# Kernel tuning notes

Hardware: AMD Instinct MI355X
Metric: run time of the kernel (lower is better)

Reference implementation:

```python
import jax, jax.numpy as jnp
import numpy as np

N_NODES = 100000
N_EDGES = 1600000
HIDDEN = 256
CONV_OUT = 128
OUT = 2


def setup_inputs() -> dict:
    key = jax.random.key(0)
    k1, k2, k3, k4, k5, k6, k7 = jax.random.split(key, 7)
    x = jax.random.normal(k1, (N_NODES, HIDDEN), dtype=jnp.float32)
    edge_index = jax.random.randint(k2, (2, N_EDGES), 0, N_NODES, dtype=jnp.int64)
    edge_weight = jax.random.uniform(k3, (N_EDGES,), dtype=jnp.float32)
    # GCNConv parameters (lin: hidden->128, bias added after aggregation)
    W1 = jax.random.normal(k4, (HIDDEN, CONV_OUT), dtype=jnp.float32) / np.sqrt(HIDDEN)
    b1 = jnp.zeros((CONV_OUT,), dtype=jnp.float32)
    # head Linear(128, out_channels)
    W2 = jax.random.normal(k5, (CONV_OUT, OUT), dtype=jnp.float32) / np.sqrt(CONV_OUT)
    b2 = jax.random.normal(k6, (OUT,), dtype=jnp.float32) * 0.01
    return {"x": x, "edge_index": edge_index, "edge_weight": edge_weight,
            "W1": W1, "b1": b1, "W2": W2, "b2": b2}


def reference(x, edge_index, edge_weight, W1, b1, W2, b2):
    # GCNConv (use_weights=True branch, no relu), dropout in eval mode (identity), then Linear.
    N = x.shape[0]
    src, dst = edge_index[0], edge_index[1]
    # add self-loops with weight 1 (PyG default fill_value=1.0)
    loop = jnp.arange(N, dtype=src.dtype)
    src = jnp.concatenate([src, loop])
    dst = jnp.concatenate([dst, loop])
    w = jnp.concatenate([edge_weight, jnp.ones((N,), dtype=edge_weight.dtype)])
    # symmetric normalization: norm = d^{-1/2}[src] * w * d^{-1/2}[dst]
    deg = jax.ops.segment_sum(w, dst, num_segments=N)
    dinv = jnp.where(deg > 0, jax.lax.rsqrt(deg), 0.0)
    norm = dinv[src] * w * dinv[dst]
    # transform then gather-scatter aggregate
    h = x @ W1                                   # [N, 128]
    msgs = norm[:, None] * h[src]                # [E+N, 128]
    agg = jax.ops.segment_sum(msgs, dst, num_segments=N) + b1  # [N, 128]
    return agg @ W2 + b2                         # [N, out_channels]
```

## Files before the change

### kernel.cpp

```cpp
#include <hip/hip_runtime.h>

#define N_NODES 100000
#define N_EDGES 1600000
#define HIDDEN 256

#define BSH 7
#define BNODES 128
#define NB 782
#define CAP 2560
#define NPB 200
#define EPB 8000
#define ZNPW 16
#define ZNPB 64
#define NZB 1563


__global__ __launch_bounds__(256) void k_init(
        const float* __restrict__ W1, const float* __restrict__ b1,
        const float* __restrict__ W2, const float* __restrict__ b2,
        float* __restrict__ W12, float* __restrict__ cvec, int* __restrict__ gcur) {
    if (blockIdx.x == 0) {
        int h = threadIdx.x;
        const float4* w1r = (const float4*)(W1 + (size_t)h * 128);
        float a0 = 0.f, a1 = 0.f;
#pragma unroll 8
        for (int k4 = 0; k4 < 32; ++k4) {
            float4 v = w1r[k4];
            a0 += v.x * W2[8 * k4 + 0]; a1 += v.x * W2[8 * k4 + 1];
            a0 += v.y * W2[8 * k4 + 2]; a1 += v.y * W2[8 * k4 + 3];
            a0 += v.z * W2[8 * k4 + 4]; a1 += v.z * W2[8 * k4 + 5];
            a0 += v.w * W2[8 * k4 + 6]; a1 += v.w * W2[8 * k4 + 7];
        }
        W12[2 * h] = a0; W12[2 * h + 1] = a1;
        if (h < 2) {
            float acc = b2[h];
            for (int k = 0; k < 128; ++k) acc += b1[k] * W2[2 * k + h];
            cvec[h] = acc;
        }
    } else {
        int i = (blockIdx.x - 1) * 256 + threadIdx.x;
        if (i < NB) gcur[i] = 0;
    }
}

__global__ __launch_bounds__(256) void k_main(
        const float* __restrict__ x, const int* __restrict__ ei,
        const float* __restrict__ ew, const float* __restrict__ W12,
        int* __restrict__ gcur, uint2* __restrict__ rec, float* __restrict__ z) {
    __shared__ struct { int hist[NB]; int cursor[NB]; } sm;
    const int tid = threadIdx.x, bid = blockIdx.x;
    if (bid < NPB) {
        for (int i = tid; i < NB; i += 256) sm.hist[i] = 0;
        __syncthreads();
        const int e0 = bid * EPB;
        for (int e = e0 + tid; e < e0 + EPB; e += 256)
            atomicAdd(&sm.hist[((unsigned)ei[N_EDGES + e]) >> BSH], 1);
        __syncthreads();
        for (int i = tid; i < NB; i += 256) {
            int c = sm.hist[i];
            int pos = c ? atomicAdd(&gcur[i], c) : 0;
            sm.cursor[i] = i * CAP + pos;
        }
        __syncthreads();
        for (int e = e0 + tid; e < e0 + EPB; e += 256) {
            int d = ei[N_EDGES + e];
            int s = ei[e];
            int bk = ((unsigned)d) >> BSH;
            int p = atomicAdd(&sm.cursor[bk], 1);
            if (p < (bk + 1) * CAP)
                rec[p] = make_uint2((unsigned)s | ((unsigned)(d & (BNODES - 1)) << 17),
                                    __float_as_uint(ew[e]));
        }
    } else {
        const int lane = tid & 63;
        const float2 w0 = ((const float2*)W12)[lane * 4 + 0];
        const float2 w1 = ((const float2*)W12)[lane * 4 + 1];
        const float2 w2 = ((const float2*)W12)[lane * 4 + 2];
        const float2 w3 = ((const float2*)W12)[lane * 4 + 3];
        const int n0 = (bid - NPB) * ZNPB + (tid >> 6) * ZNPW;
#pragma unroll 4
        for (int k = 0; k < ZNPW; ++k) {
            const int node = n0 + k;
            if (node < N_NODES) {
                float4 xv = *(const float4*)(x + (size_t)node * HIDDEN + lane * 4);
                float a0 = xv.x * w0.x + xv.y * w1.x + xv.z * w2.x + xv.w * w3.x;
                float a1 = xv.x * w0.y + xv.y * w1.y + xv.z * w2.y + xv.w * w3.y;
#pragma unroll
                for (int m = 32; m >= 1; m >>= 1) {
                    a0 += __shfl_xor(a0, m, 64);
                    a1 += __shfl_xor(a1, m, 64);
                }
                if (lane == 0) ((float2*)z)[node] = make_float2(a0, a1);
            }
        }
    }
}

__global__ __launch_bounds__(256) void k_deg(
        const uint2* __restrict__ rec, const int* __restrict__ gcur,
        const float* __restrict__ z, float* __restrict__ dinv,
        float2* __restrict__ zn) {
    __shared__ float acc[BNODES];
    const int tid = threadIdx.x, b = blockIdx.x;
    for (int i = tid; i < BNODES; i += 256) acc[i] = 1.0f;
    __syncthreads();
    const int n = min(gcur[b], CAP);
    const uint2* r = rec + (size_t)b * CAP;
    int i = tid * 2;
    for (; i + 1 < n; i += 512) {
        uint4 q = *(const uint4*)(r + i);
        atomicAdd(&acc[q.x >> 17], __uint_as_float(q.y));
        atomicAdd(&acc[q.z >> 17], __uint_as_float(q.w));
    }
    if (i < n) {
        uint2 q = r[i];
        atomicAdd(&acc[q.x >> 17], __uint_as_float(q.y));
    }
    __syncthreads();
    for (int i2 = tid; i2 < BNODES; i2 += 256) {
        int node = b * BNODES + i2;
        if (node < N_NODES) {
            float di = rsqrtf(acc[i2]);
            dinv[node] = di;
            float2 zv = ((const float2*)z)[node];
            zn[node] = make_float2(di * zv.x, di * zv.y);
        }
    }
}

__global__ __launch_bounds__(256) void k_gather(
        const uint2* __restrict__ rec, const int* __restrict__ gcur,
        const float* __restrict__ dinv, const float2* __restrict__ zn,
        const float* __restrict__ cvec, float2* __restrict__ out) {
    __shared__ float ax[BNODES], ay[BNODES];
    const int tid = threadIdx.x, b = blockIdx.x;
    for (int i = tid; i < BNODES; i += 256) { ax[i] = 0.f; ay[i] = 0.f; }
    __syncthreads();
    const int n = min(gcur[b], CAP);
    const uint2* r = rec + (size_t)b * CAP;
    int i = tid * 2;
    for (; i + 1 < n; i += 512) {
        uint4 q = *(const uint4*)(r + i);
        {
            float w = __uint_as_float(q.y);
            float2 s = zn[q.x & 0x1FFFFu];
            int dl = (int)(q.x >> 17);
            atomicAdd(&ax[dl], w * s.x);
            atomicAdd(&ay[dl], w * s.y);
        }
        {
            float w = __uint_as_float(q.w);
            float2 s = zn[q.z & 0x1FFFFu];
            int dl = (int)(q.z >> 17);
            atomicAdd(&ax[dl], w * s.x);
            atomicAdd(&ay[dl], w * s.y);
        }
    }
    if (i < n) {
        uint2 q = r[i];
        float w = __uint_as_float(q.y);
        float2 s = zn[q.x & 0x1FFFFu];
        int dl = (int)(q.x >> 17);
        atomicAdd(&ax[dl], w * s.x);
        atomicAdd(&ay[dl], w * s.y);
    }
    __syncthreads();
    const float c0 = cvec[0], c1 = cvec[1];
    for (int i2 = tid; i2 < BNODES; i2 += 256) {
        int node = b * BNODES + i2;
        if (node < N_NODES) {
            float di = dinv[node];
            float2 s = zn[node];
            out[node] = make_float2(di * ax[i2] + di * s.x + c0,
                                    di * ay[i2] + di * s.y + c1);
        }
    }
}

extern "C" void kernel_launch(void* const* d_in, const int* in_sizes, int n_in,
                              void* d_out, int out_size, void* d_ws, size_t ws_size,
                              hipStream_t stream) {
    const float* x  = (const float*)d_in[0];
    const int*   ei = (const int*)d_in[1];
    const float* ew = (const float*)d_in[2];
    const float* W1 = (const float*)d_in[3];
    const float* b1 = (const float*)d_in[4];
    const float* W2 = (const float*)d_in[5];
    const float* b2 = (const float*)d_in[6];
    float2* out = (float2*)d_out;

    char* ws = (char*)d_ws;
    uint2*  rec  = (uint2*)ws;           size_t off = (size_t)NB * CAP * 8;
    int*    gcur = (int*)(ws + off);     off += 3200;
    float*  dinv = (float*)(ws + off);   off += (size_t)N_NODES * 4;
    float*  z    = (float*)(ws + off);   off += (size_t)N_NODES * 8;
    float2* zn   = (float2*)(ws + off);  off += (size_t)N_NODES * 8;
    float*  W12  = (float*)(ws + off);   off += HIDDEN * 2 * 4;
    float*  cvec = (float*)(ws + off);   off += 16;

    k_init  <<<5, 256, 0, stream>>>(W1, b1, W2, b2, W12, cvec, gcur);
    k_main  <<<NPB + NZB, 256, 0, stream>>>(x, ei, ew, W12, gcur, rec, z);
    k_deg   <<<NB, 256, 0, stream>>>(rec, gcur, z, dinv, zn);
    k_gather<<<NB, 256, 0, stream>>>(rec, gcur, dinv, zn, cvec, out);
}
```

Measured before the change: 93.03 us.

## Register-cache edges, spread binning over more blocks, pad global bucket counters

Result: slower. 105.4 us (+13.2%).

```diff
diff --git a/kernel.cpp b/kernel.cpp
--- a/kernel.cpp
+++ b/kernel.cpp
@@ -8,11 +8,13 @@
 #define BNODES 128
 #define NB 782
 #define CAP 2560
-#define NPB 200
-#define EPB 8000
-#define ZNPW 16
-#define ZNPB 64
-#define NZB 1563
+#define NPB 512
+#define EPB 3125
+#define EPT 13
+#define GSTR 16
+#define ZNPW 8
+#define ZNPB 32
+#define NZB 3125
 
 
 __global__ __launch_bounds__(256) void k_init(
@@ -39,7 +41,7 @@
         }
     } else {
         int i = (blockIdx.x - 1) * 256 + threadIdx.x;
-        if (i < NB) gcur[i] = 0;
+        if (i < NB * GSTR) gcur[i] = 0;
     }
 }
 
@@ -50,26 +52,40 @@
     __shared__ struct { int hist[NB]; int cursor[NB]; } sm;
     const int tid = threadIdx.x, bid = blockIdx.x;
     if (bid < NPB) {
+        const int e0 = bid * EPB, e1 = e0 + EPB;
+        int dv[EPT]; int sv[EPT]; float wv[EPT];
+#pragma unroll
+        for (int k = 0; k < EPT; ++k) {
+            int e = e0 + tid + k * 256;
+            if (e < e1) {
+                dv[k] = ei[N_EDGES + e];
+                sv[k] = ei[e];
+                wv[k] = ew[e];
+            } else dv[k] = -1;
+        }
         for (int i = tid; i < NB; i += 256) sm.hist[i] = 0;
         __syncthreads();
-        const int e0 = bid * EPB;
-        for (int e = e0 + tid; e < e0 + EPB; e += 256)
-            atomicAdd(&sm.hist[((unsigned)ei[N_EDGES + e]) >> BSH], 1);
+#pragma unroll
+        for (int k = 0; k < EPT; ++k)
+            if (dv[k] >= 0) atomicAdd(&sm.hist[((unsigned)dv[k]) >> BSH], 1);
         __syncthreads();
         for (int i = tid; i < NB; i += 256) {
             int c = sm.hist[i];
-            int pos = c ? atomicAdd(&gcur[i], c) : 0;
+            int pos = c ? atomicAdd(&gcur[i * GSTR], c) : 0;
             sm.cursor[i] = i * CAP + pos;
         }
         __syncthreads();
-        for (int e = e0 + tid; e < e0 + EPB; e += 256) {
-            int d = ei[N_EDGES + e];
-            int s = ei[e];
-            int bk = ((unsigned)d) >> BSH;
-            int p = atomicAdd(&sm.cursor[bk], 1);
-            if (p < (bk + 1) * CAP)
-                rec[p] = make_uint2((unsigned)s | ((unsigned)(d & (BNODES - 1)) << 17),
-                                    __float_as_uint(ew[e]));
+#pragma unroll
+        for (int k = 0; k < EPT; ++k) {
+            if (dv[k] >= 0) {
+                int d = dv[k];
+                int bk = ((unsigned)d) >> BSH;
+                int p = atomicAdd(&sm.cursor[bk], 1);
+                if (p < (bk + 1) * CAP)
+                    rec[p] = make_uint2(
+                        (unsigned)sv[k] | ((unsigned)(d & (BNODES - 1)) << 17),
+                        __float_as_uint(wv[k]));
+            }
         }
     } else {
         const int lane = tid & 63;
@@ -81,17 +97,15 @@
 #pragma unroll 4
         for (int k = 0; k < ZNPW; ++k) {
             const int node = n0 + k;
-            if (node < N_NODES) {
-                float4 xv = *(const float4*)(x + (size_t)node * HIDDEN + lane * 4);
-                float a0 = xv.x * w0.x + xv.y * w1.x + xv.z * w2.x + xv.w * w3.x;
-                float a1 = xv.x * w0.y + xv.y * w1.y + xv.z * w2.y + xv.w * w3.y;
-#pragma unroll
-                for (int m = 32; m >= 1; m >>= 1) {
-                    a0 += __shfl_xor(a0, m, 64);
-                    a1 += __shfl_xor(a1, m, 64);
-                }
-                if (lane == 0) ((float2*)z)[node] = make_float2(a0, a1);
+            float4 xv = *(const float4*)(x + (size_t)node * HIDDEN + lane * 4);
+            float a0 = xv.x * w0.x + xv.y * w1.x + xv.z * w2.x + xv.w * w3.x;
+            float a1 = xv.x * w0.y + xv.y * w1.y + xv.z * w2.y + xv.w * w3.y;
+#pragma unroll
+            for (int m = 32; m >= 1; m >>= 1) {
+                a0 += __shfl_xor(a0, m, 64);
+                a1 += __shfl_xor(a1, m, 64);
             }
+            if (lane == 0) ((float2*)z)[node] = make_float2(a0, a1);
         }
     }
 }
@@ -104,7 +118,7 @@
     const int tid = threadIdx.x, b = blockIdx.x;
     for (int i = tid; i < BNODES; i += 256) acc[i] = 1.0f;
     __syncthreads();
-    const int n = min(gcur[b], CAP);
+    const int n = min(gcur[b * GSTR], CAP);
     const uint2* r = rec + (size_t)b * CAP;
     int i = tid * 2;
     for (; i + 1 < n; i += 512) {
@@ -136,7 +150,7 @@
     const int tid = threadIdx.x, b = blockIdx.x;
     for (int i = tid; i < BNODES; i += 256) { ax[i] = 0.f; ay[i] = 0.f; }
     __syncthreads();
-    const int n = min(gcur[b], CAP);
+    const int n = min(gcur[b * GSTR], CAP);
     const uint2* r = rec + (size_t)b * CAP;
     int i = tid * 2;
     for (; i + 1 < n; i += 512) {
@@ -191,14 +205,14 @@
 
     char* ws = (char*)d_ws;
     uint2*  rec  = (uint2*)ws;           size_t off = (size_t)NB * CAP * 8;
-    int*    gcur = (int*)(ws + off);     off += 3200;
+    int*    gcur = (int*)(ws + off);     off += (size_t)NB * GSTR * 4;
     float*  dinv = (float*)(ws + off);   off += (size_t)N_NODES * 4;
     float*  z    = (float*)(ws + off);   off += (size_t)N_NODES * 8;
     float2* zn   = (float2*)(ws + off);  off += (size_t)N_NODES * 8;
     float*  W12  = (float*)(ws + off);   off += HIDDEN * 2 * 4;
     float*  cvec = (float*)(ws + off);   off += 16;
 
-    k_init  <<<5, 256, 0, stream>>>(W1, b1, W2, b2, W12, cvec, gcur);
+    k_init  <<<1 + (NB * GSTR + 255) / 256, 256, 0, stream>>>(W1, b1, W2, b2, W12, cvec, gcur);
     k_main  <<<NPB + NZB, 256, 0, stream>>>(x, ei, ew, W12, gcur, rec, z);
     k_deg   <<<NB, 256, 0, stream>>>(rec, gcur, z, dinv, zn);
     k_gather<<<NB, 256, 0, stream>>>(rec, gcur, dinv, zn, cvec, out);
```

## Replace global-atomic bucket sort with per-block fixed-slot bucket layout

Applied to the files above, without the earlier changes.

New measurement: 88.06 us. -5.3%, faster.

```diff
diff --git a/kernel.cpp b/kernel.cpp
--- a/kernel.cpp
+++ b/kernel.cpp
@@ -7,18 +7,16 @@
 #define BSH 7
 #define BNODES 128
 #define NB 782
-#define CAP 2560
-#define NPB 200
-#define EPB 8000
-#define ZNPW 16
-#define ZNPB 64
-#define NZB 1563
+#define NPB 256
+#define EPB 6250
+#define SLOTS 32
+#define NZB 25000
 
 
 __global__ __launch_bounds__(256) void k_init(
         const float* __restrict__ W1, const float* __restrict__ b1,
         const float* __restrict__ W2, const float* __restrict__ b2,
-        float* __restrict__ W12, float* __restrict__ cvec, int* __restrict__ gcur) {
+        float* __restrict__ W12, float* __restrict__ cvec, int* __restrict__ cnt) {
     if (blockIdx.x == 0) {
         int h = threadIdx.x;
         const float4* w1r = (const float4*)(W1 + (size_t)h * 128);
@@ -39,82 +37,70 @@
         }
     } else {
         int i = (blockIdx.x - 1) * 256 + threadIdx.x;
-        if (i < NB) gcur[i] = 0;
+        if (i < NPB * NB) cnt[i] = 0;
     }
 }
 
 __global__ __launch_bounds__(256) void k_main(
         const float* __restrict__ x, const int* __restrict__ ei,
         const float* __restrict__ ew, const float* __restrict__ W12,
-        int* __restrict__ gcur, uint2* __restrict__ rec, float* __restrict__ z) {
-    __shared__ struct { int hist[NB]; int cursor[NB]; } sm;
+        int* __restrict__ cnt, uint2* __restrict__ rec, float* __restrict__ z) {
+    __shared__ int cursor[NB];
     const int tid = threadIdx.x, bid = blockIdx.x;
     if (bid < NPB) {
-        for (int i = tid; i < NB; i += 256) sm.hist[i] = 0;
+        for (int i = tid; i < NB; i += 256) cursor[i] = 0;
         __syncthreads();
-        const int e0 = bid * EPB;
-        for (int e = e0 + tid; e < e0 + EPB; e += 256)
-            atomicAdd(&sm.hist[((unsigned)ei[N_EDGES + e]) >> BSH], 1);
-        __syncthreads();
-        for (int i = tid; i < NB; i += 256) {
-            int c = sm.hist[i];
-            int pos = c ? atomicAdd(&gcur[i], c) : 0;
-            sm.cursor[i] = i * CAP + pos;
+        const int e0 = bid * EPB, e1 = e0 + EPB;
+        for (int e = e0 + tid; e < e1; e += 256) {
+            int d = ei[N_EDGES + e];
+            int s = ei[e];
+            float wv = ew[e];
+            int bk = ((unsigned)d) >> BSH;
+            int pos = atomicAdd(&cursor[bk], 1);
+            if (pos < SLOTS)
+                rec[((size_t)bk * NPB + bid) * SLOTS + pos] =
+                    make_uint2((unsigned)s | ((unsigned)(d & (BNODES - 1)) << 17),
+                               __float_as_uint(wv));
         }
         __syncthreads();
-        for (int e = e0 + tid; e < e0 + EPB; e += 256) {
-            int d = ei[N_EDGES + e];
-            int s = ei[e];
-            int bk = ((unsigned)d) >> BSH;
-            int p = atomicAdd(&sm.cursor[bk], 1);
-            if (p < (bk + 1) * CAP)
-                rec[p] = make_uint2((unsigned)s | ((unsigned)(d & (BNODES - 1)) << 17),
-                                    __float_as_uint(ew[e]));
-        }
+        for (int i = tid; i < NB; i += 256)
+            cnt[bid * NB + i] = min(cursor[i], SLOTS);
     } else {
         const int lane = tid & 63;
         const float2 w0 = ((const float2*)W12)[lane * 4 + 0];
         const float2 w1 = ((const float2*)W12)[lane * 4 + 1];
         const float2 w2 = ((const float2*)W12)[lane * 4 + 2];
         const float2 w3 = ((const float2*)W12)[lane * 4 + 3];
-        const int n0 = (bid - NPB) * ZNPB + (tid >> 6) * ZNPW;
-#pragma unroll 4
-        for (int k = 0; k < ZNPW; ++k) {
-            const int node = n0 + k;
-            if (node < N_NODES) {
-                float4 xv = *(const float4*)(x + (size_t)node * HIDDEN + lane * 4);
-                float a0 = xv.x * w0.x + xv.y * w1.x + xv.z * w2.x + xv.w * w3.x;
-                float a1 = xv.x * w0.y + xv.y * w1.y + xv.z * w2.y + xv.w * w3.y;
+        const int node = (bid - NPB) * 4 + (tid >> 6);
+        float4 xv = *(const float4*)(x + (size_t)node * HIDDEN + lane * 4);
+        float a0 = xv.x * w0.x + xv.y * w1.x + xv.z * w2.x + xv.w * w3.x;
+        float a1 = xv.x * w0.y + xv.y * w1.y + xv.z * w2.y + xv.w * w3.y;
 #pragma unroll
-                for (int m = 32; m >= 1; m >>= 1) {
-                    a0 += __shfl_xor(a0, m, 64);
-                    a1 += __shfl_xor(a1, m, 64);
-                }
-                if (lane == 0) ((float2*)z)[node] = make_float2(a0, a1);
-            }
+        for (int m = 32; m >= 1; m >>= 1) {
+            a0 += __shfl_xor(a0, m, 64);
+            a1 += __shfl_xor(a1, m, 64);
         }
+        if (lane == 0) ((float2*)z)[node] = make_float2(a0, a1);
     }
 }
 
 __global__ __launch_bounds__(256) void k_deg(
-        const uint2* __restrict__ rec, const int* __restrict__ gcur,
+        const uint2* __restrict__ rec, const int* __restrict__ cnt,
         const float* __restrict__ z, float* __restrict__ dinv,
         float2* __restrict__ zn) {
     __shared__ float acc[BNODES];
+    __shared__ int csh[NPB];
     const int tid = threadIdx.x, b = blockIdx.x;
     for (int i = tid; i < BNODES; i += 256) acc[i] = 1.0f;
+    csh[tid] = cnt[tid * NB + b];
     __syncthreads();
-    const int n = min(gcur[b], CAP);
-    const uint2* r = rec + (size_t)b * CAP;
-    int i = tid * 2;
-    for (; i + 1 < n; i += 512) {
-        uint4 q = *(const uint4*)(r + i);
-        atomicAdd(&acc[q.x >> 17], __uint_as_float(q.y));
-        atomicAdd(&acc[q.z >> 17], __uint_as_float(q.w));
-    }
-    if (i < n) {
-        uint2 q = r[i];
-        atomicAdd(&acc[q.x >> 17], __uint_as_float(q.y));
+    const uint2* r = rec + (size_t)b * NPB * SLOTS;
+    for (int idx = tid; idx < NPB * SLOTS; idx += 256) {
+        int j = idx >> 5, s2 = idx & (SLOTS - 1);
+        if (s2 < csh[j]) {
+            uint2 q = r[idx];
+            atomicAdd(&acc[q.x >> 17], __uint_as_float(q.y));
+        }
     }
     __syncthreads();
     for (int i2 = tid; i2 < BNODES; i2 += 256) {
@@ -129,40 +115,26 @@
 }
 
 __global__ __launch_bounds__(256) void k_gather(
-        const uint2* __restrict__ rec, const int* __restrict__ gcur,
+        const uint2* __restrict__ rec, const int* __restrict__ cnt,
         const float* __restrict__ dinv, const float2* __restrict__ zn,
         const float* __restrict__ cvec, float2* __restrict__ out) {
     __shared__ float ax[BNODES], ay[BNODES];
+    __shared__ int csh[NPB];
     const int tid = threadIdx.x, b = blockIdx.x;
     for (int i = tid; i < BNODES; i += 256) { ax[i] = 0.f; ay[i] = 0.f; }
+    csh[tid] = cnt[tid * NB + b];
     __syncthreads();
-    const int n = min(gcur[b], CAP);
-    const uint2* r = rec + (size_t)b * CAP;
-    int i = tid * 2;
-    for (; i + 1 < n; i += 512) {
-        uint4 q = *(const uint4*)(r + i);
-        {
+    const uint2* r = rec + (size_t)b * NPB * SLOTS;
+    for (int idx = tid; idx < NPB * SLOTS; idx += 256) {
+        int j = idx >> 5, s2 = idx & (SLOTS - 1);
+        if (s2 < csh[j]) {
+            uint2 q = r[idx];
             float w = __uint_as_float(q.y);
             float2 s = zn[q.x & 0x1FFFFu];
             int dl = (int)(q.x >> 17);
             atomicAdd(&ax[dl], w * s.x);
             atomicAdd(&ay[dl], w * s.y);
         }
-        {
-            float w = __uint_as_float(q.w);
-            float2 s = zn[q.z & 0x1FFFFu];
-            int dl = (int)(q.z >> 17);
-            atomicAdd(&ax[dl], w * s.x);
-            atomicAdd(&ay[dl], w * s.y);
-        }
-    }
-    if (i < n) {
-        uint2 q = r[i];
-        float w = __uint_as_float(q.y);
-        float2 s = zn[q.x & 0x1FFFFu];
-        int dl = (int)(q.x >> 17);
-        atomicAdd(&ax[dl], w * s.x);
-        atomicAdd(&ay[dl], w * s.y);
     }
     __syncthreads();
     const float c0 = cvec[0], c1 = cvec[1];
@@ -190,16 +162,16 @@
     float2* out = (float2*)d_out;
 
     char* ws = (char*)d_ws;
-    uint2*  rec  = (uint2*)ws;           size_t off = (size_t)NB * CAP * 8;
-    int*    gcur = (int*)(ws + off);     off += 3200;
+    uint2*  rec  = (uint2*)ws;           size_t off = (size_t)NB * NPB * SLOTS * 8;
+    int*    cnt  = (int*)(ws + off);     off += (size_t)NPB * NB * 4;
     float*  dinv = (float*)(ws + off);   off += (size_t)N_NODES * 4;
     float*  z    = (float*)(ws + off);   off += (size_t)N_NODES * 8;
     float2* zn   = (float2*)(ws + off);  off += (size_t)N_NODES * 8;
     float*  W12  = (float*)(ws + off);   off += HIDDEN * 2 * 4;
     float*  cvec = (float*)(ws + off);   off += 16;
 
-    k_init  <<<5, 256, 0, stream>>>(W1, b1, W2, b2, W12, cvec, gcur);
-    k_main  <<<NPB + NZB, 256, 0, stream>>>(x, ei, ew, W12, gcur, rec, z);
-    k_deg   <<<NB, 256, 0, stream>>>(rec, gcur, z, dinv, zn);
-    k_gather<<<NB, 256, 0, stream>>>(rec, gcur, dinv, zn, cvec, out);
+    k_init  <<<1 + (NPB * NB + 255) / 256, 256, 0, stream>>>(W1, b1, W2, b2, W12, cvec, cnt);
+    k_main  <<<NPB + NZB, 256, 0, stream>>>(x, ei, ew, W12, cnt, rec, z);
+    k_deg   <<<NB, 256, 0, stream>>>(rec, cnt, z, dinv, zn);
+    k_gather<<<NB, 256, 0, stream>>>(rec, cnt, dinv, zn, cvec, out);
 }
```
